# Optimization experiments

Measured on AMD Instinct MI355X. Metric: run time of the kernel, lower is better.

The kernel has to match this reference:

```python
import jax, jax.numpy as jnp
import numpy as np

# dims / hyperparams (match init_kwargs)
B, C, H, W = 1, 48, 160, 160
COUT = 48
RANK = 12
K = 8          # topK neighbors
WS = 32        # window_size
KS = 3         # local conv kernel / local mask size
M = 3          # circ_rows
DELTA = 10.0
LEAK = 0.01


def circ_dense(x, w, m):
    """CircDense: x (N, Cin), w (Cout//m, 1, Cin) -> (N, Cout).
    Equivalent to circular-pad + conv1d in the torch module."""
    cin = x.shape[1]
    xp = jnp.concatenate([x, x[:, : m - 1]], axis=1)            # circular pad to Cin+m-1
    xw = jnp.stack([xp[:, j : j + cin] for j in range(m)], 1)   # (N, m, Cin)
    out = jnp.einsum('njc,ic->nij', xw, w[:, 0, :])             # (N, Cout//m, m)
    return out.reshape(x.shape[0], -1)


def windowed_topk(h, k, ws, ks):
    """knn.windowedTopK: per 32x32 window, K nearest neighbors by feature L2,
    excluding the ks x ks local neighborhood (localMask). Returns (B,K,H,W)
    global flat pixel indices."""
    b, c, hh, ww = h.shape
    nh, nw = hh // ws, ww // ws
    ws2 = ws * ws
    hw = h.reshape(b, c, nh, ws, nw, ws).transpose(0, 2, 4, 3, 5, 1)
    hw = hw.reshape(b, nh, nw, ws2, c)                          # windowed features
    sq = jnp.sum(hw * hw, -1)
    d = sq[..., :, None] + sq[..., None, :] - 2.0 * jnp.einsum('bijnc,bijmc->bijnm', hw, hw)
    r = jnp.arange(ws2) // ws
    cc = jnp.arange(ws2) % ws
    loc = (jnp.abs(r[:, None] - r[None, :]) <= ks // 2) & (jnp.abs(cc[:, None] - cc[None, :]) <= ks // 2)
    d = jnp.where(loc, 1e10, d)                                 # mask local neighborhood
    _, idx = jax.lax.top_k(-d, k)                               # (b,nh,nw,ws2,k) local idx
    wi = jnp.arange(nh)[:, None, None, None]
    wj = jnp.arange(nw)[None, :, None, None]
    g = (wi * ws + idx // ws) * ww + (wj * ws + idx % ws)       # global flat idx
    g = g.reshape(b, nh, nw, ws, ws, k).transpose(0, 5, 1, 3, 2, 4).reshape(b, k, hh, ww)
    return g


def low_rank_ecc(h, edge, W0, b0, WL, WR, Wk, bk):
    b, k, hh, ww = edge.shape
    n = hh * ww
    cin = h.shape[1]
    hf = h.reshape(b, cin, n)
    ef = edge.reshape(b, k, n)
    # gather neighbor (vertex) features: (b, cin, k, n) -> (b, k, n, cin)
    vertex = jax.vmap(lambda hb, eb: hb[:, eb])(hf, ef).transpose(0, 2, 3, 1)
    center = hf.transpose(0, 2, 1)[:, None]                     # (b,1,n,cin)
    label = vertex - center                                     # edge labels
    lt = label.reshape(-1, cin)                                 # (B0, Cin), B0=b*k*n
    vt = vertex.reshape(-1, cin)
    theta = jax.nn.leaky_relu(lt @ W0.T + b0, LEAK)
    tL = circ_dense(theta, WL, M).reshape(-1, COUT, RANK)       # (B0, Cout, rank)
    tR = circ_dense(theta, WR, M).reshape(-1, cin, RANK)        # (B0, Cin, rank)
    kap = theta @ Wk.T + bk                                     # (B0, rank)
    tmp = kap * jnp.einsum('bcr,bc->br', tR, vt)                # thetaR^T @ v, scaled
    out = jnp.einsum('bor,br->bo', tL, tmp)                     # thetaL @ (...)
    gamma = jnp.exp(-jnp.sum(lt * lt, 1, keepdims=True) / DELTA)
    out = (gamma * out).reshape(b, k, n, COUT).mean(1)          # mean over K neighbors
    return out.transpose(0, 2, 1).reshape(b, COUT, hh, ww)


def local_conv(h, w):
    p = KS // 2
    hp = jnp.pad(h, ((0, 0), (0, 0), (p, p), (p, p)), mode='reflect')
    return jax.lax.conv_general_dilated(hp, w, (1, 1), 'VALID',
                                        dimension_numbers=('NCHW', 'OIHW', 'NCHW'))


def setup_inputs() -> dict:
    key = jax.random.key(0)
    ks_ = jax.random.split(key, 9)
    s_in = 1.0 / np.sqrt(C)
    return {
        'h': jax.random.normal(ks_[0], (B, C, H, W), jnp.float32),
        'W0': jax.random.normal(ks_[1], (C, C), jnp.float32) * s_in,
        'b0': jnp.zeros((C,), jnp.float32),
        'WL': jax.random.normal(ks_[2], (RANK * COUT // M, 1, C), jnp.float32) * s_in,
        'WR': jax.random.normal(ks_[3], (RANK * C // M, 1, C), jnp.float32) * s_in,
        'Wk': jax.random.normal(ks_[4], (RANK, C), jnp.float32) * s_in,
        'bk': jnp.zeros((RANK,), jnp.float32),
        'Wconv': jax.random.normal(ks_[5], (COUT, C, KS, KS), jnp.float32) * (1.0 / np.sqrt(C * KS * KS)),
        'bias': jnp.zeros((1, COUT, 1, 1), jnp.float32),
    }


def reference(h, W0, b0, WL, WR, Wk, bk, Wconv, bias):
    edge = windowed_topk(h, K, WS, KS)
    hNL = low_rank_ecc(h, edge, W0, b0, WL, WR, Wk, bk)
    hL = local_conv(h, Wconv)
    return (hNL + hL) / 2.0 + bias
```

## Files before the change

### kernel.cpp

```cpp
#include <hip/hip_runtime.h>

#define CC    48
#define HH    160
#define WWID  160
#define NPIX  25600
#define KK    8

typedef unsigned short u16;
typedef unsigned int u32;
typedef __attribute__((ext_vector_type(8))) short bf16x8;
typedef __attribute__((ext_vector_type(4))) float f32x4;

__device__ __forceinline__ float bf2f(u16 u) {
    return __uint_as_float(((unsigned int)u) << 16);
}
__device__ __forceinline__ u16 f2bf(float f) {
    unsigned int x = __float_as_uint(f);
    return (u16)((x + 0x7FFFu + ((x >> 16) & 1u)) >> 16);
}

#define OFF_B0    0
#define OFF_BK    48
#define OFF_WKT   60
#define OFF_WBH   636
#define OFF_WBL   8828
#define OFF_WLH   17020
#define OFF_WLL   21628
#define OFF_SQP   26236
#define OFF_W0V   51836
#define OFF_VTB   1280636
#define OFF_HHT   3738236
#define OFF_HLT   4557436
#define OFF_PARTK 5376636
#define OFF_UBAR  7015036

__global__ void prep_kernel(const float* W0, const float* b0, const float* WL,
                            const float* WR, const float* Wk, const float* bk,
                            float* ws) {
    float* b0f = ws + OFF_B0;
    float* bkf = ws + OFF_BK;
    float* wkt = ws + OFF_WKT;
    u16*   wbh = (u16*)(ws + OFF_WBH);
    u16*   wbl = (u16*)(ws + OFF_WBL);
    u16*   wlh = (u16*)(ws + OFF_WLH);
    u16*   wll = (u16*)(ws + OFF_WLL);
    int t = blockIdx.x * 256 + threadIdx.x;
    int stride = gridDim.x * 256;
    for (int i = t; i < 16384; i += stride) {
        int col = i >> 6, k = i & 63;
        float v = 0.f;
        if (k < 48) {
            if (col < 192)      v = WR[(4*k + (col & 3))*48 + (col >> 2)];
            else if (col < 240) v = W0[(col - 192)*48 + k];
        }
        u16 hi = f2bf(v);
        wbh[i] = hi;
        wbl[i] = f2bf(v - bf2f(hi));
    }
    for (int i = t; i < 9216; i += stride) {
        int o = i / 192, k = i % 192;
        float v = WL[(4*o + (k & 3))*48 + (k >> 2)];
        u16 hi = f2bf(v);
        wlh[i] = hi;
        wll[i] = f2bf(v - bf2f(hi));
    }
    for (int i = t; i < 576; i += stride) { int c = i / 12, r = i % 12; wkt[i] = Wk[r*48 + c]; }
    for (int i = t; i < 48; i += stride) { b0f[i] = b0[i]; }
    for (int i = t; i < 12; i += stride) { bkf[i] = bk[i]; }
}

__global__ __launch_bounds__(256) void split_kernel(const float* h, float* sqp,
                                                    u16* hht, u16* hlt) {
    int tid = threadIdx.x;
    int p = blockIdx.x * 128 + (tid >> 1);
    int half = tid & 1;
    float sq = 0.f;
    u16 hh[24], hl[24];
    #pragma unroll
    for (int i = 0; i < 24; i++) {
        int c = half*24 + i;
        float v = h[c*NPIX + p];
        sq = fmaf(v, v, sq);
        u16 hi = f2bf(v);
        hh[i] = hi;
        hl[i] = f2bf(v - bf2f(hi));
    }
    sq += __shfl_xor(sq, 1, 64);
    if (half == 0) sqp[p] = sq;
    uint4* dh = (uint4*)&hht[(long)p*64 + half*24];
    uint4* dl = (uint4*)&hlt[(long)p*64 + half*24];
    const uint4* s1 = (const uint4*)hh;
    const uint4* s2 = (const uint4*)hl;
    dh[0] = s1[0]; dh[1] = s1[1]; dh[2] = s1[2];
    dl[0] = s2[0]; dl[1] = s2[1]; dl[2] = s2[2];
    if (half) {
        uint4 z = make_uint4(0, 0, 0, 0);
        uint4* zh = (uint4*)&hht[(long)p*64 + 48];
        uint4* zl = (uint4*)&hlt[(long)p*64 + 48];
        zh[0] = z; zh[1] = z;
        zl[0] = z; zl[1] = z;
    }
}

__global__ __launch_bounds__(512) void pixvt_mfma(const u16* hht, const u16* hlt,
                                                  const float* ws, float* w0v, u16* vtb) {
    __shared__ __align__(16) char smem[38912];
    u16*   a_hi = (u16*)smem;
    u16*   a_lo = (u16*)(smem + 8192);
    u16*   vt_s = (u16*)smem;
    float* w0_s = (float*)(smem + 25600);

    const u16* wbh = (const u16*)(ws + OFF_WBH);
    const u16* wbl = (const u16*)(ws + OFF_WBL);

    int tid = threadIdx.x;
    int pbase = blockIdx.x * 64;

    {
        int blk = tid >> 6, row = tid & 63;
        int swz = (blk ^ (row & 7)) * 8;
        *(uint4*)&a_hi[row*64 + swz] = *(const uint4*)&hht[(long)(pbase + row)*64 + blk*8];
        *(uint4*)&a_lo[row*64 + swz] = *(const uint4*)&hlt[(long)(pbase + row)*64 + blk*8];
    }
    __syncthreads();

    int w = tid >> 6, lane = tid & 63;
    int lm = lane & 15, lg = lane >> 4;
    int c2a = 2*w, c2b = 2*w + 1;

    f32x4 acc0[4], acc1[4];
    #pragma unroll
    for (int t = 0; t < 4; t++) { acc0[t] = (f32x4){0.f,0.f,0.f,0.f}; acc1[t] = (f32x4){0.f,0.f,0.f,0.f}; }

    #pragma unroll
    for (int s = 0; s < 2; s++) {
        int lblk = 4*s + lg;
        int aswz = (lblk ^ (lm & 7)) * 8;
        bf16x8 ah0 = *(const bf16x8*)&a_hi[( 0 + lm)*64 + aswz];
        bf16x8 ah1 = *(const bf16x8*)&a_hi[(16 + lm)*64 + aswz];
        bf16x8 ah2 = *(const bf16x8*)&a_hi[(32 + lm)*64 + aswz];
        bf16x8 ah3 = *(const bf16x8*)&a_hi[(48 + lm)*64 + aswz];
        bf16x8 al0 = *(const bf16x8*)&a_lo[( 0 + lm)*64 + aswz];
        bf16x8 al1 = *(const bf16x8*)&a_lo[(16 + lm)*64 + aswz];
        bf16x8 al2 = *(const bf16x8*)&a_lo[(32 + lm)*64 + aswz];
        bf16x8 al3 = *(const bf16x8*)&a_lo[(48 + lm)*64 + aswz];
        {
            int col = c2a*16 + lm;
            bf16x8 bh = *(const bf16x8*)&wbh[col*64 + lblk*8];
            bf16x8 bl = *(const bf16x8*)&wbl[col*64 + lblk*8];
            acc0[0] = __builtin_amdgcn_mfma_f32_16x16x32_bf16(ah0, bh, acc0[0], 0, 0, 0);
            acc0[0] = __builtin_amdgcn_mfma_f32_16x16x32_bf16(ah0, bl, acc0[0], 0, 0, 0);
            acc0[0] = __builtin_amdgcn_mfma_f32_16x16x32_bf16(al0, bh, acc0[0], 0, 0, 0);
            acc0[1] = __builtin_amdgcn_mfma_f32_16x16x32_bf16(ah1, bh, acc0[1], 0, 0, 0);
            acc0[1] = __builtin_amdgcn_mfma_f32_16x16x32_bf16(ah1, bl, acc0[1], 0, 0, 0);
            acc0[1] = __builtin_amdgcn_mfma_f32_16x16x32_bf16(al1, bh, acc0[1], 0, 0, 0);
            acc0[2] = __builtin_amdgcn_mfma_f32_16x16x32_bf16(ah2, bh, acc0[2], 0, 0, 0);
            acc0[2] = __builtin_amdgcn_mfma_f32_16x16x32_bf16(ah2, bl, acc0[2], 0, 0, 0);
            acc0[2] = __builtin_amdgcn_mfma_f32_16x16x32_bf16(al2, bh, acc0[2], 0, 0, 0);
            acc0[3] = __builtin_amdgcn_mfma_f32_16x16x32_bf16(ah3, bh, acc0[3], 0, 0, 0);
            acc0[3] = __builtin_amdgcn_mfma_f32_16x16x32_bf16(ah3, bl, acc0[3], 0, 0, 0);
            acc0[3] = __builtin_amdgcn_mfma_f32_16x16x32_bf16(al3, bh, acc0[3], 0, 0, 0);
        }
        if (c2b < 15) {
            int col = c2b*16 + lm;
            bf16x8 bh = *(const bf16x8*)&wbh[col*64 + lblk*8];
            bf16x8 bl = *(const bf16x8*)&wbl[col*64 + lblk*8];
            acc1[0] = __builtin_amdgcn_mfma_f32_16x16x32_bf16(ah0, bh, acc1[0], 0, 0, 0);
            acc1[0] = __builtin_amdgcn_mfma_f32_16x16x32_bf16(ah0, bl, acc1[0], 0, 0, 0);
            acc1[0] = __builtin_amdgcn_mfma_f32_16x16x32_bf16(al0, bh, acc1[0], 0, 0, 0);
            acc1[1] = __builtin_amdgcn_mfma_f32_16x16x32_bf16(ah1, bh, acc1[1], 0, 0, 0);
            acc1[1] = __builtin_amdgcn_mfma_f32_16x16x32_bf16(ah1, bl, acc1[1], 0, 0, 0);
            acc1[1] = __builtin_amdgcn_mfma_f32_16x16x32_bf16(al1, bh, acc1[1], 0, 0, 0);
            acc1[2] = __builtin_amdgcn_mfma_f32_16x16x32_bf16(ah2, bh, acc1[2], 0, 0, 0);
            acc1[2] = __builtin_amdgcn_mfma_f32_16x16x32_bf16(ah2, bl, acc1[2], 0, 0, 0);
            acc1[2] = __builtin_amdgcn_mfma_f32_16x16x32_bf16(al2, bh, acc1[2], 0, 0, 0);
            acc1[3] = __builtin_amdgcn_mfma_f32_16x16x32_bf16(ah3, bh, acc1[3], 0, 0, 0);
            acc1[3] = __builtin_amdgcn_mfma_f32_16x16x32_bf16(ah3, bl, acc1[3], 0, 0, 0);
            acc1[3] = __builtin_amdgcn_mfma_f32_16x16x32_bf16(al3, bh, acc1[3], 0, 0, 0);
        }
    }
    __syncthreads();

    {
        int col = c2a*16 + lm;
        if (c2a < 12) {
            #pragma unroll
            for (int t = 0; t < 4; t++)
                #pragma unroll
                for (int r = 0; r < 4; r++)
                    vt_s[(t*16 + lg*4 + r)*200 + col] = f2bf(acc0[t][r]);
        } else {
            int o = col - 192;
            #pragma unroll
            for (int t = 0; t < 4; t++)
                #pragma unroll
                for (int r = 0; r < 4; r++)
                    w0_s[(t*16 + lg*4 + r)*52 + o] = acc0[t][r];
        }
    }
    if (c2b < 15) {
        int col = c2b*16 + lm;
        if (c2b < 12) {
            #pragma unroll
            for (int t = 0; t < 4; t++)
                #pragma unroll
                for (int r = 0; r < 4; r++)
                    vt_s[(t*16 + lg*4 + r)*200 + col] = f2bf(acc1[t][r]);
        } else {
            int o = col - 192;
            #pragma unroll
            for (int t = 0; t < 4; t++)
                #pragma unroll
                for (int r = 0; r < 4; r++)
                    w0_s[(t*16 + lg*4 + r)*52 + o] = acc1[t][r];
        }
    }
    __syncthreads();

    {
        int px = tid >> 3, c8 = tid & 7;
        #pragma unroll
        for (int j = 0; j < 3; j++) {
            int ch = c8 + 8*j;
            uint4 v = *(const uint4*)&vt_s[px*200 + ch*8];
            *(uint4*)&vtb[(long)(pbase + px)*192 + ch*8] = v;
        }
        float* dst = w0v + (long)(pbase + px)*48 + c8*6;
        const float* src = w0_s + px*52 + c8*6;
        #pragma unroll
        for (int k = 0; k < 3; k++) {
            float2 v2 = *(const float2*)&src[k*2];
            *(float2*)&dst[k*2] = v2;
        }
    }
}

__global__ __launch_bounds__(512, 8) void topk_mfma(const u16* hht, const u16* hlt,
                                                    const float* sqp, u32* partk) {
    __shared__ u16 ca_hi[128*64];
    __shared__ u16 ca_lo[128*64];
    __shared__ float sq_s[128];

    int tid = threadIdx.x;
    int b = (blockIdx.x & 7) * 200 + (blockIdx.x >> 3);
    int chunk = b & 7, pg = (b >> 3) & 7, win = b >> 6;
    int wi = win / 5, wj = win % 5;
    int base = wi*32*WWID + wj*32;

    #pragma unroll
    for (int r = 0; r < 2; r++) {
        int task = r*512 + tid;
        int blk = task >> 7, row = task & 127;
        int swz = (blk ^ (row & 7)) * 8;
        int ml = chunk*128 + row;
        long gp = base + (ml>>5)*WWID + (ml&31);
        *(uint4*)&ca_hi[row*64 + swz] = *(const uint4*)&hht[gp*64 + blk*8];
        *(uint4*)&ca_lo[row*64 + swz] = *(const uint4*)&hlt[gp*64 + blk*8];
    }
    if (tid < 128) {
        int ml = chunk*128 + tid;
        sq_s[tid] = sqp[base + (ml>>5)*WWID + (ml&31)];
    }
    __syncthreads();

    int w = tid >> 6, lane = tid & 63;
    int lm = lane & 15, lg = lane >> 4;

    int nl = pg*128 + w*16 + lm;
    long gpx = base + (nl>>5)*WWID + (nl&31);

    f32x4 acc[8];
    #pragma unroll
    for (int t = 0; t < 8; t++) acc[t] = (f32x4){0.f, 0.f, 0.f, 0.f};

    #pragma unroll
    for (int s = 0; s < 2; s++) {
        int lblk = 4*s + lg;
        int ko = lblk * 8;
        bf16x8 bh = *(const bf16x8*)&hht[gpx*64 + ko];
        bf16x8 bl = *(const bf16x8*)&hlt[gpx*64 + ko];
        #pragma unroll
        for (int t = 0; t < 8; t++) {
            int aoff = (t*16 + lm)*64 + (lblk ^ (lm & 7))*8;
            bf16x8 ah = *(const bf16x8*)&ca_hi[aoff];
            bf16x8 al = *(const bf16x8*)&ca_lo[aoff];
            acc[t] = __builtin_amdgcn_mfma_f32_16x16x32_bf16(ah, bh, acc[t], 0, 0, 0);
            acc[t] = __builtin_amdgcn_mfma_f32_16x16x32_bf16(ah, bl, acc[t], 0, 0, 0);
            acc[t] = __builtin_amdgcn_mfma_f32_16x16x32_bf16(al, bh, acc[t], 0, 0, 0);
        }
    }

    int rn = nl >> 5, cn = nl & 31;
    int rowok[8], colok[8];
    #pragma unroll
    for (int t = 0; t < 8; t++) {
        int rm = chunk*4 + (t >> 1);
        int dr = rn - rm; dr = dr < 0 ? -dr : dr;
        rowok[t] = (dr <= 1);
    }
    #pragma unroll
    for (int j = 0; j < 8; j++) {
        int cm = (j >> 2)*16 + lg*4 + (j & 3);
        int dc = cn - cm; dc = dc < 0 ? -dc : dc;
        colok[j] = (dc <= 1);
    }

    u32 k8[8];
    #pragma unroll
    for (int s = 0; s < 8; s++) k8[s] = 0xFFFFFFFFu;

    #pragma unroll
    for (int t = 0; t < 8; t++) {
        #pragma unroll
        for (int r = 0; r < 4; r++) {
            int cl = t*16 + lg*4 + r;
            int ml = chunk*128 + cl;
            float d = fmaf(-2.0f, acc[t][r], sq_s[cl]);
            u32 u = __float_as_uint(d);
            u32 key = u ^ (0x80000000u | (u32)((int)u >> 31));
            key = (key & 0xFFFFFC00u) | (u32)ml;
            bool bad = rowok[t] && colok[(t & 1)*4 + r];
            key = bad ? 0xFFFFFFFFu : key;
            #pragma unroll
            for (int s = 0; s < 8; s++) {
                u32 lo = min(k8[s], key);
                u32 hi = max(k8[s], key);
                k8[s] = lo; key = hi;
            }
        }
    }

    #pragma unroll
    for (int st = 0; st < 2; st++) {
        int mk = (st == 0) ? 16 : 32;
        u32 o[8];
        #pragma unroll
        for (int s = 0; s < 8; s++) o[s] = (u32)__shfl_xor((int)k8[s], mk, 64);
        u32 c0 = min(k8[0], o[7]);
        u32 c1 = min(k8[1], o[6]);
        u32 c2 = min(k8[2], o[5]);
        u32 c3 = min(k8[3], o[4]);
        u32 c4 = min(k8[4], o[3]);
        u32 c5 = min(k8[5], o[2]);
        u32 c6 = min(k8[6], o[1]);
        u32 c7 = min(k8[7], o[0]);
        u32 a, bb;
        a = min(c0,c4); bb = max(c0,c4); c0 = a; c4 = bb;
        a = min(c1,c5); bb = max(c1,c5); c1 = a; c5 = bb;
        a = min(c2,c6); bb = max(c2,c6); c2 = a; c6 = bb;
        a = min(c3,c7); bb = max(c3,c7); c3 = a; c7 = bb;
        a = min(c0,c2); bb = max(c0,c2); c0 = a; c2 = bb;
        a = min(c1,c3); bb = max(c1,c3); c1 = a; c3 = bb;
        a = min(c4,c6); bb = max(c4,c6); c4 = a; c6 = bb;
        a = min(c5,c7); bb = max(c5,c7); c5 = a; c7 = bb;
        a = min(c0,c1); bb = max(c0,c1); c0 = a; c1 = bb;
        a = min(c2,c3); bb = max(c2,c3); c2 = a; c3 = bb;
        a = min(c4,c5); bb = max(c4,c5); c4 = a; c5 = bb;
        a = min(c6,c7); bb = max(c6,c7); c6 = a; c7 = bb;
        k8[0]=c0; k8[1]=c1; k8[2]=c2; k8[3]=c3; k8[4]=c4; k8[5]=c5; k8[6]=c6; k8[7]=c7;
    }

    {
        int n = base + (nl >> 5)*WWID + (nl & 31);
        u32 v0, v1;
        if      (lg == 0) { v0 = k8[0]; v1 = k8[1]; }
        else if (lg == 1) { v0 = k8[2]; v1 = k8[3]; }
        else if (lg == 2) { v0 = k8[4]; v1 = k8[5]; }
        else              { v0 = k8[6]; v1 = k8[7]; }
        u32* pk = partk + (long)chunk*8*NPIX + (long)(2*lg)*NPIX + n;
        pk[0]    = v0;
        pk[NPIX] = v1;
    }
}

__global__ __launch_bounds__(128, 4) void ecc_kernel(const float* ws, const u32* partk,
                                                     const u16* vtb, u16* ubar) {
    const float* b0f = ws + OFF_B0;
    const float* bkf = ws + OFF_BK;
    const float* wkt = ws + OFF_WKT;
    const float* w0v = ws + OFF_W0V;
    const float* sqp = ws + OFF_SQP;

    __shared__ u16 th_s[128][50];

    int tid = threadIdx.x;
    int sb = (blockIdx.x & 7) * 200 + (blockIdx.x >> 3);
    int pix = tid >> 3, sh = tid & 7;
    int n = sb * 16 + pix;

    u32 k8[8];
    {
        const u32* pk = partk + (long)sh*8*NPIX + n;
        #pragma unroll
        for (int s = 0; s < 8; s++) k8[s] = pk[(long)s*NPIX];
    }
    #pragma unroll
    for (int st = 0; st < 3; st++) {
        int mk = 1 << st;
        u32 o[8];
        #pragma unroll
        for (int s = 0; s < 8; s++) o[s] = (u32)__shfl_xor((int)k8[s], mk, 64);
        u32 c0 = min(k8[0], o[7]);
        u32 c1 = min(k8[1], o[6]);
        u32 c2 = min(k8[2], o[5]);
        u32 c3 = min(k8[3], o[4]);
        u32 c4 = min(k8[4], o[3]);
        u32 c5 = min(k8[5], o[2]);
        u32 c6 = min(k8[6], o[1]);
        u32 c7 = min(k8[7], o[0]);
        u32 a, bb;
        a = min(c0,c4); bb = max(c0,c4); c0 = a; c4 = bb;
        a = min(c1,c5); bb = max(c1,c5); c1 = a; c5 = bb;
        a = min(c2,c6); bb = max(c2,c6); c2 = a; c6 = bb;
        a = min(c3,c7); bb = max(c3,c7); c3 = a; c7 = bb;
        a = min(c0,c2); bb = max(c0,c2); c0 = a; c2 = bb;
        a = min(c1,c3); bb = max(c1,c3); c1 = a; c3 = bb;
        a = min(c4,c6); bb = max(c4,c6); c4 = a; c6 = bb;
        a = min(c5,c7); bb = max(c5,c7); c5 = a; c7 = bb;
        a = min(c0,c1); bb = max(c0,c1); c0 = a; c1 = bb;
        a = min(c2,c3); bb = max(c2,c3); c2 = a; c3 = bb;
        a = min(c4,c5); bb = max(c4,c5); c4 = a; c5 = bb;
        a = min(c6,c7); bb = max(c6,c7); c6 = a; c7 = bb;
        k8[0]=c0; k8[1]=c1; k8[2]=c2; k8[3]=c3; k8[4]=c4; k8[5]=c5; k8[6]=c6; k8[7]=c7;
    }
    u32 key;
    {
        u32 m0 = (sh & 1) ? k8[1] : k8[0];
        u32 m1 = (sh & 1) ? k8[3] : k8[2];
        u32 m2 = (sh & 1) ? k8[5] : k8[4];
        u32 m3 = (sh & 1) ? k8[7] : k8[6];
        u32 n0 = (sh & 2) ? m1 : m0;
        u32 n1 = (sh & 2) ? m3 : m2;
        key = (sh & 4) ? n1 : n0;
    }
    int ml = (int)(key & 1023u);
    u32 uf = key & 0xFFFFFC00u;
    u32 uu = (uf & 0x80000000u) ? (uf ^ 0x80000000u) : ~uf;
    float d = __uint_as_float(uu);
    int y = n / WWID, x = n % WWID;
    int wy = (y >> 5) << 5, wx = (x >> 5) << 5;
    int m = (wy + (ml >> 5)) * WWID + (wx + (ml & 31));
    float gamma = expf(-(d + sqp[n]) * 0.1f);

    float th[48];
    {
        const float4* wm4 = (const float4*)(w0v + (long)m * 48);
        const float4* wn4 = (const float4*)(w0v + (long)n * 48);
        #pragma unroll
        for (int i = 0; i < 12; i++) {
            float4 a = wm4[i];
            float4 b = wn4[i];
            float x0 = a.x - b.x + b0f[4*i+0];
            float x1 = a.y - b.y + b0f[4*i+1];
            float x2 = a.z - b.z + b0f[4*i+2];
            float x3 = a.w - b.w + b0f[4*i+3];
            th[4*i+0] = (x0 >= 0.f) ? x0 : 0.01f * x0;
            th[4*i+1] = (x1 >= 0.f) ? x1 : 0.01f * x1;
            th[4*i+2] = (x2 >= 0.f) ? x2 : 0.01f * x2;
            th[4*i+3] = (x3 >= 0.f) ? x3 : 0.01f * x3;
        }
    }

    #pragma unroll
    for (int i = 0; i < 24; i++) {
        ushort2 pr;
        pr.x = f2bf(th[2*i]);
        pr.y = f2bf(th[2*i+1]);
        *(ushort2*)&th_s[tid][2*i] = pr;
    }

    float kap[12];
    #pragma unroll
    for (int r = 0; r < 12; r++) kap[r] = bkf[r];
    #pragma unroll
    for (int c = 0; c < 48; c++) {
        float t = th[c];
        const float* wkc = wkt + c*12;
        #pragma unroll
        for (int r = 0; r < 12; r++) kap[r] = fmaf(wkc[r], t, kap[r]);
    }

    float sr[12];
    #pragma unroll
    for (int r = 0; r < 12; r++) sr[r] = 0.f;
    const u16* vrow = vtb + (long)m * 192;
    #pragma unroll
    for (int j = 0; j < 24; j++) {
        uint4 vv = *(const uint4*)&vrow[j*8];
        #pragma unroll
        for (int half = 0; half < 2; half++) {
            int cp = 2*j + half;
            u32 w0_ = half ? vv.z : vv.x;
            u32 w1_ = half ? vv.w : vv.y;
            float vx = bf2f((u16)(w0_ & 0xffff));
            float vy = bf2f((u16)(w0_ >> 16));
            float vz = bf2f((u16)(w1_ & 0xffff));
            float vw = bf2f((u16)(w1_ >> 16));
            int i1 = (cp + 1 < 48) ? cp + 1 : cp - 47;
            int i2 = (cp + 2 < 48) ? cp + 2 : cp - 46;
            float t0 = th[cp], t1 = th[i1], t2 = th[i2];
            sr[0] = fmaf(t0, vx, sr[0]); sr[1]  = fmaf(t1, vx, sr[1]);  sr[2]  = fmaf(t2, vx, sr[2]);
            sr[3] = fmaf(t0, vy, sr[3]); sr[4]  = fmaf(t1, vy, sr[4]);  sr[5]  = fmaf(t2, vy, sr[5]);
            sr[6] = fmaf(t0, vz, sr[6]); sr[7]  = fmaf(t1, vz, sr[7]);  sr[8]  = fmaf(t2, vz, sr[8]);
            sr[9] = fmaf(t0, vw, sr[9]); sr[10] = fmaf(t1, vw, sr[10]); sr[11] = fmaf(t2, vw, sr[11]);
        }
    }

    float tmp[12];
    #pragma unroll
    for (int r = 0; r < 12; r++) tmp[r] = kap[r] * sr[r];

    __syncthreads();

    float acc0[6], acc1[6], acc2[6], acc3[6];
    #pragma unroll
    for (int j = 0; j < 6; j++) { acc0[j] = 0.f; acc1[j] = 0.f; acc2[j] = 0.f; acc3[j] = 0.f; }
    #pragma unroll 1
    for (int e = 0; e < 8; e++) {
        int srcl = (tid & 56) + e;
        int row  = (tid & 120) + e;
        float tm[12];
        #pragma unroll
        for (int r = 0; r < 12; r++) tm[r] = __shfl(tmp[r], srcl, 64);
        float ge = __shfl(gamma, srcl, 64);
        #pragma unroll
        for (int j = 0; j < 6; j++) {
            int cp = sh + 8*j;
            int i1 = (cp + 1 < 48) ? cp + 1 : cp - 47;
            int i2 = (cp + 2 < 48) ? cp + 2 : cp - 46;
            float t0 = bf2f(th_s[row][cp]);
            float t1 = bf2f(th_s[row][i1]);
            float t2 = bf2f(th_s[row][i2]);
            float u0 = tm[0]*t0 + tm[1]*t1 + tm[2]*t2;
            float u1 = tm[3]*t0 + tm[4]*t1 + tm[5]*t2;
            float u2 = tm[6]*t0 + tm[7]*t1 + tm[8]*t2;
            float u3 = tm[9]*t0 + tm[10]*t1 + tm[11]*t2;
            acc0[j] = fmaf(ge, u0, acc0[j]);
            acc1[j] = fmaf(ge, u1, acc1[j]);
            acc2[j] = fmaf(ge, u2, acc2[j]);
            acc3[j] = fmaf(ge, u3, acc3[j]);
        }
    }
    u16* ub = ubar + (long)n * 192;
    #pragma unroll
    for (int j = 0; j < 6; j++) {
        int cp = sh + 8*j;
        ushort4 st;
        st.x = f2bf(acc0[j]); st.y = f2bf(acc1[j]);
        st.z = f2bf(acc2[j]); st.w = f2bf(acc3[j]);
        *(ushort4*)&ub[cp*4] = st;
    }
}

__global__ __launch_bounds__(256) void wl_mfma(const float* ws, const u16* ubar, float* outp) {
    __shared__ __align__(16) char smem[25600];
    u16*   a_s = (u16*)smem;
    float* c_s = (float*)smem;

    const u16* wlh = (const u16*)(ws + OFF_WLH);
    const u16* wll = (const u16*)(ws + OFF_WLL);

    int tid = threadIdx.x;
    int pbase = blockIdx.x * 64;

    #pragma unroll
    for (int i = 0; i < 6; i++) {
        int task = i*256 + tid;
        int px = task / 24, ch = task % 24;
        *(uint4*)&a_s[px*200 + ch*8] = *(const uint4*)&ubar[(long)(pbase + px)*192 + ch*8];
    }
    __syncthreads();

    int w = tid >> 6, lane = tid & 63;
    int lm = lane & 15, lg = lane >> 4;

    f32x4 acc[3];
    #pragma unroll
    for (int t = 0; t < 3; t++) acc[t] = (f32x4){0.f, 0.f, 0.f, 0.f};

    #pragma unroll
    for (int ks = 0; ks < 6; ks++) {
        bf16x8 a = *(const bf16x8*)&a_s[(w*16 + lm)*200 + ks*32 + lg*8];
        #pragma unroll
        for (int ct = 0; ct < 3; ct++) {
            int col = ct*16 + lm;
            bf16x8 bh = *(const bf16x8*)&wlh[col*192 + ks*32 + lg*8];
            bf16x8 bl = *(const bf16x8*)&wll[col*192 + ks*32 + lg*8];
            acc[ct] = __builtin_amdgcn_mfma_f32_16x16x32_bf16(a, bh, acc[ct], 0, 0, 0);
            acc[ct] = __builtin_amdgcn_mfma_f32_16x16x32_bf16(a, bl, acc[ct], 0, 0, 0);
        }
    }
    __syncthreads();

    #pragma unroll
    for (int ct = 0; ct < 3; ct++) {
        int o = ct*16 + lm;
        #pragma unroll
        for (int r = 0; r < 4; r++)
            c_s[o*68 + w*16 + lg*4 + r] = 0.0625f * acc[ct][r];
    }
    __syncthreads();

    #pragma unroll
    for (int j = 0; j < 12; j++) {
        int idx = j*256 + tid;
        int o = idx >> 6, px = idx & 63;
        outp[(long)o*NPIX + pbase + px] = c_s[o*68 + px];
    }
}

#define OCH 4
__global__ __launch_bounds__(320) void conv_kernel(const float* h, const float* wc,
                                                   const float* bias, float* outp) {
    int sb = (blockIdx.x & 7) * 120 + (blockIdx.x >> 3);
    int og = sb % 12;
    int yp = sb / 12;
    int t  = threadIdx.x;
    int ty = t / 160;
    int x  = t % 160;
    int y  = yp * 2 + ty;

    int idx9[9];
    #pragma unroll
    for (int dy = 0; dy < 3; dy++) {
        int yy = y + dy - 1;
        yy = yy < 0 ? -yy : (yy >= HH ? 2*HH - 2 - yy : yy);
        #pragma unroll
        for (int dx = 0; dx < 3; dx++) {
            int xx = x + dx - 1;
            xx = xx < 0 ? -xx : (xx >= WWID ? 2*WWID - 2 - xx : xx);
            idx9[dy*3 + dx] = yy * WWID + xx;
        }
    }

    float acc[OCH];
    #pragma unroll
    for (int oi = 0; oi < OCH; oi++) acc[oi] = 0.f;

    const float* wbase = wc + og * OCH * 432;
    for (int c = 0; c < 48; c++) {
        float v[9];
        #pragma unroll
        for (int k = 0; k < 9; k++) v[k] = h[c*NPIX + idx9[k]];
        #pragma unroll
        for (int oi = 0; oi < OCH; oi++) {
            const float* w9 = wbase + oi*432 + c*9;
            float a = acc[oi];
            a = fmaf(v[0], w9[0], a);
            a = fmaf(v[1], w9[1], a);
            a = fmaf(v[2], w9[2], a);
            a = fmaf(v[3], w9[3], a);
            a = fmaf(v[4], w9[4], a);
            a = fmaf(v[5], w9[5], a);
            a = fmaf(v[6], w9[6], a);
            a = fmaf(v[7], w9[7], a);
            a = fmaf(v[8], w9[8], a);
            acc[oi] = a;
        }
    }

    int p = y * WWID + x;
    #pragma unroll
    for (int oi = 0; oi < OCH; oi++) {
        int o = og * OCH + oi;
        outp[o*NPIX + p] = outp[o*NPIX + p] + 0.5f * acc[oi] + bias[o];
    }
}

extern "C" void kernel_launch(void* const* d_in, const int* in_sizes, int n_in,
                              void* d_out, int out_size, void* d_ws, size_t ws_size,
                              hipStream_t stream) {
    const float* h    = (const float*)d_in[0];
    const float* W0   = (const float*)d_in[1];
    const float* b0   = (const float*)d_in[2];
    const float* WL   = (const float*)d_in[3];
    const float* WR   = (const float*)d_in[4];
    const float* Wk   = (const float*)d_in[5];
    const float* bk   = (const float*)d_in[6];
    const float* Wc   = (const float*)d_in[7];
    const float* bias = (const float*)d_in[8];

    float* ws     = (float*)d_ws;
    float* sqp    = ws + OFF_SQP;
    float* w0v    = ws + OFF_W0V;
    u16*   vtb    = (u16*)(ws + OFF_VTB);
    u16*   hht    = (u16*)(ws + OFF_HHT);
    u16*   hlt    = (u16*)(ws + OFF_HLT);
    u32*   partk  = (u32*)(ws + OFF_PARTK);
    u16*   ubar   = (u16*)(ws + OFF_UBAR);
    float* outp   = (float*)d_out;

    prep_kernel<<<dim3(16), dim3(256), 0, stream>>>(W0, b0, WL, WR, Wk, bk, ws);
    split_kernel<<<dim3(200), dim3(256), 0, stream>>>(h, sqp, hht, hlt);
    topk_mfma<<<dim3(1600), dim3(512), 0, stream>>>(hht, hlt, sqp, partk);
    pixvt_mfma<<<dim3(400), dim3(512), 0, stream>>>(hht, hlt, ws, w0v, vtb);
    ecc_kernel<<<dim3(1600), dim3(128), 0, stream>>>(ws, partk, vtb, ubar);
    wl_mfma<<<dim3(400), dim3(256), 0, stream>>>(ws, ubar, outp);
    conv_kernel<<<dim3(960), dim3(320), 0, stream>>>(h, Wc, bias, outp);
}
```

Before: 143.5 us.

## Fuse WL projection MFMA into ECC kernel and prefetch vertex rows

```diff
diff --git a/kernel.cpp b/kernel.cpp
--- a/kernel.cpp
+++ b/kernel.cpp
@@ -32,7 +32,6 @@
 #define OFF_HHT   3738236
 #define OFF_HLT   4557436
 #define OFF_PARTK 5376636
-#define OFF_UBAR  7015036
 
 __global__ void prep_kernel(const float* W0, const float* b0, const float* WL,
                             const float* WR, const float* Wk, const float* bk,
@@ -374,14 +373,17 @@
 }
 
 __global__ __launch_bounds__(128, 4) void ecc_kernel(const float* ws, const u32* partk,
-                                                     const u16* vtb, u16* ubar) {
+                                                     const u16* vtb, float* outp) {
     const float* b0f = ws + OFF_B0;
     const float* bkf = ws + OFF_BK;
     const float* wkt = ws + OFF_WKT;
     const float* w0v = ws + OFF_W0V;
     const float* sqp = ws + OFF_SQP;
+    const u16*   wlh = (const u16*)(ws + OFF_WLH);
+    const u16*   wll = (const u16*)(ws + OFF_WLL);
 
     __shared__ u16 th_s[128][50];
+    __shared__ __align__(16) u16 ub_s[16*200];
 
     int tid = threadIdx.x;
     int sb = (blockIdx.x & 7) * 200 + (blockIdx.x >> 3);
@@ -442,6 +444,11 @@
     int m = (wy + (ml >> 5)) * WWID + (wx + (ml & 31));
     float gamma = expf(-(d + sqp[n]) * 0.1f);
 
+    const u16* vrow = vtb + (long)m * 192;
+    uint4 vv[8];
+    #pragma unroll
+    for (int jj = 0; jj < 8; jj++) vv[jj] = *(const uint4*)&vrow[jj*8];
+
     float th[48];
     {
         const float4* wm4 = (const float4*)(w0v + (long)m * 48);
@@ -483,26 +490,33 @@
     float sr[12];
     #pragma unroll
     for (int r = 0; r < 12; r++) sr[r] = 0.f;
-    const u16* vrow = vtb + (long)m * 192;
-    #pragma unroll
-    for (int j = 0; j < 24; j++) {
-        uint4 vv = *(const uint4*)&vrow[j*8];
-        #pragma unroll
-        for (int half = 0; half < 2; half++) {
-            int cp = 2*j + half;
-            u32 w0_ = half ? vv.z : vv.x;
-            u32 w1_ = half ? vv.w : vv.y;
-            float vx = bf2f((u16)(w0_ & 0xffff));
-            float vy = bf2f((u16)(w0_ >> 16));
-            float vz = bf2f((u16)(w1_ & 0xffff));
-            float vw = bf2f((u16)(w1_ >> 16));
-            int i1 = (cp + 1 < 48) ? cp + 1 : cp - 47;
-            int i2 = (cp + 2 < 48) ? cp + 2 : cp - 46;
-            float t0 = th[cp], t1 = th[i1], t2 = th[i2];
-            sr[0] = fmaf(t0, vx, sr[0]); sr[1]  = fmaf(t1, vx, sr[1]);  sr[2]  = fmaf(t2, vx, sr[2]);
-            sr[3] = fmaf(t0, vy, sr[3]); sr[4]  = fmaf(t1, vy, sr[4]);  sr[5]  = fmaf(t2, vy, sr[5]);
-            sr[6] = fmaf(t0, vz, sr[6]); sr[7]  = fmaf(t1, vz, sr[7]);  sr[8]  = fmaf(t2, vz, sr[8]);
-            sr[9] = fmaf(t0, vw, sr[9]); sr[10] = fmaf(t1, vw, sr[10]); sr[11] = fmaf(t2, vw, sr[11]);
+    #pragma unroll
+    for (int ch = 0; ch < 3; ch++) {
+        if (ch > 0) {
+            #pragma unroll
+            for (int jj = 0; jj < 8; jj++) vv[jj] = *(const uint4*)&vrow[(ch*8 + jj)*8];
+        }
+        #pragma unroll
+        for (int jj = 0; jj < 8; jj++) {
+            int j = ch*8 + jj;
+            uint4 v4 = vv[jj];
+            #pragma unroll
+            for (int half = 0; half < 2; half++) {
+                int cp = 2*j + half;
+                u32 w0_ = half ? v4.z : v4.x;
+                u32 w1_ = half ? v4.w : v4.y;
+                float vx = bf2f((u16)(w0_ & 0xffff));
+                float vy = bf2f((u16)(w0_ >> 16));
+                float vz = bf2f((u16)(w1_ & 0xffff));
+                float vw = bf2f((u16)(w1_ >> 16));
+                int i1 = (cp + 1 < 48) ? cp + 1 : cp - 47;
+                int i2 = (cp + 2 < 48) ? cp + 2 : cp - 46;
+                float t0 = th[cp], t1 = th[i1], t2 = th[i2];
+                sr[0] = fmaf(t0, vx, sr[0]); sr[1]  = fmaf(t1, vx, sr[1]);  sr[2]  = fmaf(t2, vx, sr[2]);
+                sr[3] = fmaf(t0, vy, sr[3]); sr[4]  = fmaf(t1, vy, sr[4]);  sr[5]  = fmaf(t2, vy, sr[5]);
+                sr[6] = fmaf(t0, vz, sr[6]); sr[7]  = fmaf(t1, vz, sr[7]);  sr[8]  = fmaf(t2, vz, sr[8]);
+                sr[9] = fmaf(t0, vw, sr[9]); sr[10] = fmaf(t1, vw, sr[10]); sr[11] = fmaf(t2, vw, sr[11]);
+            }
         }
     }
 
@@ -541,71 +555,61 @@
             acc3[j] = fmaf(ge, u3, acc3[j]);
         }
     }
-    u16* ub = ubar + (long)n * 192;
-    #pragma unroll
-    for (int j = 0; j < 6; j++) {
-        int cp = sh + 8*j;
-        ushort4 st;
-        st.x = f2bf(acc0[j]); st.y = f2bf(acc1[j]);
-        st.z = f2bf(acc2[j]); st.w = f2bf(acc3[j]);
-        *(ushort4*)&ub[cp*4] = st;
-    }
-}
-
-__global__ __launch_bounds__(256) void wl_mfma(const float* ws, const u16* ubar, float* outp) {
-    __shared__ __align__(16) char smem[25600];
-    u16*   a_s = (u16*)smem;
-    float* c_s = (float*)smem;
-
-    const u16* wlh = (const u16*)(ws + OFF_WLH);
-    const u16* wll = (const u16*)(ws + OFF_WLL);
-
-    int tid = threadIdx.x;
-    int pbase = blockIdx.x * 64;
-
-    #pragma unroll
-    for (int i = 0; i < 6; i++) {
-        int task = i*256 + tid;
-        int px = task / 24, ch = task % 24;
-        *(uint4*)&a_s[px*200 + ch*8] = *(const uint4*)&ubar[(long)(pbase + px)*192 + ch*8];
+    {
+        u16* ub = &ub_s[pix*200];
+        #pragma unroll
+        for (int j = 0; j < 6; j++) {
+            int cp = sh + 8*j;
+            ushort4 st;
+            st.x = f2bf(acc0[j]); st.y = f2bf(acc1[j]);
+            st.z = f2bf(acc2[j]); st.w = f2bf(acc3[j]);
+            *(ushort4*)&ub[cp*4] = st;
+        }
     }
     __syncthreads();
 
-    int w = tid >> 6, lane = tid & 63;
-    int lm = lane & 15, lg = lane >> 4;
-
-    f32x4 acc[3];
-    #pragma unroll
-    for (int t = 0; t < 3; t++) acc[t] = (f32x4){0.f, 0.f, 0.f, 0.f};
-
-    #pragma unroll
-    for (int ks = 0; ks < 6; ks++) {
-        bf16x8 a = *(const bf16x8*)&a_s[(w*16 + lm)*200 + ks*32 + lg*8];
-        #pragma unroll
-        for (int ct = 0; ct < 3; ct++) {
-            int col = ct*16 + lm;
-            bf16x8 bh = *(const bf16x8*)&wlh[col*192 + ks*32 + lg*8];
-            bf16x8 bl = *(const bf16x8*)&wll[col*192 + ks*32 + lg*8];
-            acc[ct] = __builtin_amdgcn_mfma_f32_16x16x32_bf16(a, bh, acc[ct], 0, 0, 0);
-            acc[ct] = __builtin_amdgcn_mfma_f32_16x16x32_bf16(a, bl, acc[ct], 0, 0, 0);
-        }
-    }
-    __syncthreads();
-
-    #pragma unroll
-    for (int ct = 0; ct < 3; ct++) {
-        int o = ct*16 + lm;
-        #pragma unroll
-        for (int r = 0; r < 4; r++)
-            c_s[o*68 + w*16 + lg*4 + r] = 0.0625f * acc[ct][r];
-    }
-    __syncthreads();
-
-    #pragma unroll
-    for (int j = 0; j < 12; j++) {
-        int idx = j*256 + tid;
-        int o = idx >> 6, px = idx & 63;
-        outp[(long)o*NPIX + pbase + px] = c_s[o*68 + px];
+    {
+        int w2 = tid >> 6;
+        int lane = tid & 63;
+        int lm = lane & 15, lg = lane >> 4;
+        int nb = sb * 16;
+        if (w2 == 0) {
+            f32x4 a0 = (f32x4){0.f,0.f,0.f,0.f};
+            f32x4 a1 = (f32x4){0.f,0.f,0.f,0.f};
+            #pragma unroll
+            for (int ks = 0; ks < 6; ks++) {
+                bf16x8 a = *(const bf16x8*)&ub_s[lm*200 + ks*32 + lg*8];
+                bf16x8 bh0 = *(const bf16x8*)&wlh[( 0 + lm)*192 + ks*32 + lg*8];
+                bf16x8 bl0 = *(const bf16x8*)&wll[( 0 + lm)*192 + ks*32 + lg*8];
+                bf16x8 bh1 = *(const bf16x8*)&wlh[(16 + lm)*192 + ks*32 + lg*8];
+                bf16x8 bl1 = *(const bf16x8*)&wll[(16 + lm)*192 + ks*32 + lg*8];
+                a0 = __builtin_amdgcn_mfma_f32_16x16x32_bf16(a, bh0, a0, 0, 0, 0);
+                a0 = __builtin_amdgcn_mfma_f32_16x16x32_bf16(a, bl0, a0, 0, 0, 0);
+                a1 = __builtin_amdgcn_mfma_f32_16x16x32_bf16(a, bh1, a1, 0, 0, 0);
+                a1 = __builtin_amdgcn_mfma_f32_16x16x32_bf16(a, bl1, a1, 0, 0, 0);
+            }
+            #pragma unroll
+            for (int r = 0; r < 4; r++) {
+                int px = lg*4 + r;
+                outp[(long)( 0 + lm)*NPIX + nb + px] = 0.0625f * a0[r];
+                outp[(long)(16 + lm)*NPIX + nb + px] = 0.0625f * a1[r];
+            }
+        } else {
+            f32x4 a2 = (f32x4){0.f,0.f,0.f,0.f};
+            #pragma unroll
+            for (int ks = 0; ks < 6; ks++) {
+                bf16x8 a = *(const bf16x8*)&ub_s[lm*200 + ks*32 + lg*8];
+                bf16x8 bh2 = *(const bf16x8*)&wlh[(32 + lm)*192 + ks*32 + lg*8];
+                bf16x8 bl2 = *(const bf16x8*)&wll[(32 + lm)*192 + ks*32 + lg*8];
+                a2 = __builtin_amdgcn_mfma_f32_16x16x32_bf16(a, bh2, a2, 0, 0, 0);
+                a2 = __builtin_amdgcn_mfma_f32_16x16x32_bf16(a, bl2, a2, 0, 0, 0);
+            }
+            #pragma unroll
+            for (int r = 0; r < 4; r++) {
+                int px = lg*4 + r;
+                outp[(long)(32 + lm)*NPIX + nb + px] = 0.0625f * a2[r];
+            }
+        }
     }
 }
 
@@ -687,14 +691,12 @@
     u16*   hht    = (u16*)(ws + OFF_HHT);
     u16*   hlt    = (u16*)(ws + OFF_HLT);
     u32*   partk  = (u32*)(ws + OFF_PARTK);
-    u16*   ubar   = (u16*)(ws + OFF_UBAR);
     float* outp   = (float*)d_out;
 
     prep_kernel<<<dim3(16), dim3(256), 0, stream>>>(W0, b0, WL, WR, Wk, bk, ws);
     split_kernel<<<dim3(200), dim3(256), 0, stream>>>(h, sqp, hht, hlt);
     topk_mfma<<<dim3(1600), dim3(512), 0, stream>>>(hht, hlt, sqp, partk);
     pixvt_mfma<<<dim3(400), dim3(512), 0, stream>>>(hht, hlt, ws, w0v, vtb);
-    ecc_kernel<<<dim3(1600), dim3(128), 0, stream>>>(ws, partk, vtb, ubar);
-    wl_mfma<<<dim3(400), dim3(256), 0, stream>>>(ws, ubar, outp);
+    ecc_kernel<<<dim3(1600), dim3(128), 0, stream>>>(ws, partk, vtb, outp);
     conv_kernel<<<dim3(960), dim3(320), 0, stream>>>(h, Wc, bias, outp);
 }
```

Measured after the change: 132.2 us, median of 3. -7.9%, faster.
